# Performance work log

Hardware: AMD Instinct MI355X
Metric: run time of the kernel (lower is better)

## Reference

```python
import jax, jax.numpy as jnp
import numpy as np

WINDOW_SIZE = 11
SIGMA = 1.5
CHANNELS = 3
DATA_RANGE = 1.0


def _create_window(window_size, channel):
    x = np.arange(window_size) - window_size // 2
    g = np.exp(-(x ** 2) / (2.0 * SIGMA ** 2))
    g = g / g.sum()
    w2d = np.outer(g, g).astype(np.float32)  # [ws, ws]
    # depthwise kernel, OIHW with I=1, O=channel
    return jnp.asarray(np.broadcast_to(w2d, (channel, 1, window_size, window_size)).copy())


def _depthwise_conv(x, window, channel):
    # x: [B, C, H, W], window: [C, 1, ws, ws], VALID padding, groups=C
    return jax.lax.conv_general_dilated(
        x, window, window_strides=(1, 1), padding='VALID',
        dimension_numbers=('NCHW', 'OIHW', 'NCHW'),
        feature_group_count=channel)


def setup_inputs() -> dict:
    key = jax.random.key(0)
    k1, k2 = jax.random.split(key)
    img1 = jax.random.uniform(k1, (32, CHANNELS, 512, 512), dtype=jnp.float32)
    img2 = jax.random.uniform(k2, (32, CHANNELS, 512, 512), dtype=jnp.float32)
    return {"img1": img1, "img2": img2}


def reference(img1, img2):
    channel = img1.shape[1]
    window = _create_window(WINDOW_SIZE, channel).astype(img1.dtype)

    mu1 = _depthwise_conv(img1, window, channel)
    mu2 = _depthwise_conv(img2, window, channel)
    mu1_sq = mu1 * mu1
    mu2_sq = mu2 * mu2
    mu1_mu2 = mu1 * mu2

    sigma1_sq = _depthwise_conv(img1 * img1, window, channel) - mu1_sq
    sigma2_sq = _depthwise_conv(img2 * img2, window, channel) - mu2_sq
    sigma12 = _depthwise_conv(img1 * img2, window, channel) - mu1_mu2

    C1 = (0.01 * DATA_RANGE) ** 2
    C2 = (0.03 * DATA_RANGE) ** 2
    v1 = 2.0 * sigma12 + C2
    v2 = sigma1_sq + sigma2_sq + C2
    ssim_map = (2.0 * mu1_mu2 + C1) * v1 / ((mu1_sq + mu2_sq + C1) * v2)
    # mean over channel, height, width -> per-image SSIM [B]
    return ssim_map.mean(axis=(1, 2, 3))
```

## Files before the change

### kernel.cpp

```cpp
#include <hip/hip_runtime.h>
#include <math.h>

#define H 512
#define W 512
#define OUT_H 502
#define OUT_W 502
#define C1c 1.0e-4f
#define C2c 9.0e-4f

#define TH 111
#define NR 121
#define NCOLS 256
#define HALO 10
#define RING_W 266

__global__ __launch_bounds__(256, 4)
void ssim_kernel(const float* __restrict__ img1,
                 const float* __restrict__ img2,
                 float* __restrict__ out) {
    __shared__ float2 ring[2][RING_W];
    __shared__ float wsum[4];

    const int tid = threadIdx.x;

    float g[11];
    {
        float s = 0.f;
#pragma unroll
        for (int i = 0; i < 11; ++i) {
            float d = (float)(i - 5);
            g[i] = expf(-d * d * (1.0f / 4.5f));
            s += g[i];
        }
        float inv = 1.0f / s;
#pragma unroll
        for (int i = 0; i < 11; ++i) {
            g[i] *= inv;
            g[i] = __uint_as_float(__builtin_amdgcn_readfirstlane(__float_as_uint(g[i])));
        }
    }

    const int X0  = blockIdx.x * NCOLS;
    const int oyb = blockIdx.y * TH;
    const int Y0  = min(oyb, H - NR);
    const int plane = blockIdx.z;
    const size_t pbase = (size_t)plane * (H * W);
    const float* __restrict__ p1 = img1 + pbase;
    const float* __restrict__ p2 = img2 + pbase;

    const int gx = X0 + tid;
    const int hx = min(X0 + NCOLS + tid, W - 1);
    const bool colok = (gx < OUT_W);

    float a0[11], a1[11], a2[11], a3[11], a4[11];
#pragma unroll
    for (int i = 0; i < 11; ++i) { a0[i]=0.f; a1[i]=0.f; a2[i]=0.f; a3[i]=0.f; a4[i]=0.f; }

    float lsum = 0.f;

    int rowoff = Y0 * W;
    const int rowcap = (H - 1) * W;

    float va, vb, ha = 0.f, hb = 0.f;
    {
        const float* row1 = p1 + rowoff;
        const float* row2 = p2 + rowoff;
        va = row1[gx]; vb = row2[gx];
        if (tid < HALO) { ha = row1[hx]; hb = row2[hx]; }
    }

#pragma unroll 1
    for (int rb = 0; rb < NR; rb += 11) {
#pragma unroll
        for (int p = 0; p < 11; ++p) {
            const int r = rb + p;
            float2* rs = ring[r & 1];

            rs[tid] = make_float2(va, vb);
            if (tid < HALO) rs[NCOLS + tid] = make_float2(ha, hb);

            __syncthreads();

            rowoff = min(rowoff + W, rowcap);
            {
                const float* row1 = p1 + rowoff;
                const float* row2 = p2 + rowoff;
                va = row1[gx]; vb = row2[gx];
                if (tid < HALO) { ha = row1[hx]; hb = row2[hx]; }
            }

            float h0, h1, h2, h3, h4;
            {
                const float2* rp = rs + tid;
#pragma unroll
                for (int t = 0; t < 11; ++t) {
                    const float2 v = rp[t];
                    const float w = g[t];
                    const float q2 = v.x * v.x, q3 = v.y * v.y, q4 = v.x * v.y;
                    if (t == 0) {
                        h0 = w * v.x; h1 = w * v.y; h2 = w * q2; h3 = w * q3; h4 = w * q4;
                    } else {
                        h0 = fmaf(w, v.x, h0); h1 = fmaf(w, v.y, h1);
                        h2 = fmaf(w, q2, h2);  h3 = fmaf(w, q3, h3);
                        h4 = fmaf(w, q4, h4);
                    }
                }
            }

#pragma unroll
            for (int a = 0; a < 11; ++a) {
                const float w = g[(p - a + 11) % 11];
                if (a == p) {
                    a0[a] = w * h0; a1[a] = w * h1; a2[a] = w * h2;
                    a3[a] = w * h3; a4[a] = w * h4;
                } else {
                    a0[a] = fmaf(w, h0, a0[a]); a1[a] = fmaf(w, h1, a1[a]);
                    a2[a] = fmaf(w, h2, a2[a]); a3[a] = fmaf(w, h3, a3[a]);
                    a4[a] = fmaf(w, h4, a4[a]);
                }
            }

            if (r >= 10) {
                const int e = (p + 1) % 11;
                const int oy = Y0 + r - 10;
                if (oy >= oyb) {
                    const float m1 = a0[e], m2 = a1[e];
                    const float m1s = m1 * m1, m2s = m2 * m2, m12 = m1 * m2;
                    const float sig1  = a2[e] - m1s;
                    const float sig2  = a3[e] - m2s;
                    const float sig12 = a4[e] - m12;
                    const float num = (2.f * m12 + C1c) * (2.f * sig12 + C2c);
                    const float den = (m1s + m2s + C1c) * (sig1 + sig2 + C2c);
                    const float v = num * __builtin_amdgcn_rcpf(den);
                    if (colok) lsum += v;
                }
            }
        }
    }

#pragma unroll
    for (int off = 32; off > 0; off >>= 1) lsum += __shfl_down(lsum, off, 64);
    if ((tid & 63) == 0) wsum[tid >> 6] = lsum;
    __syncthreads();
    if (tid == 0) {
        const float inv_count = 1.0f / (3.0f * (float)OUT_H * (float)OUT_W);
        const float total = (wsum[0] + wsum[1] + wsum[2] + wsum[3]) * inv_count;
        atomicAdd(&out[plane / 3], total);
    }
}

__global__ void zero_out(float* out, int n) {
    int i = threadIdx.x + blockIdx.x * blockDim.x;
    if (i < n) out[i] = 0.f;
}

extern "C" void kernel_launch(void* const* d_in, const int* in_sizes, int n_in,
                              void* d_out, int out_size, void* d_ws, size_t ws_size,
                              hipStream_t stream) {
    const float* img1 = (const float*)d_in[0];
    const float* img2 = (const float*)d_in[1];
    float* out = (float*)d_out;

    zero_out<<<1, 64, 0, stream>>>(out, out_size);

    const int nplanes = in_sizes[0] / (H * W);
    dim3 grid(W / NCOLS,
              (OUT_H + TH - 1) / TH,
              nplanes);
    ssim_kernel<<<grid, 256, 0, stream>>>(img1, img2, out);
}
```

Measured before the change: 275.2 us.

## Give each wavefront a private staging row and drop block-wide barriers

Each of the four wavefronts now owns a 64-column strip with its own 10-column halo in a private shared-memory slot. This replaces the block-wide __syncthreads per row with wave-level barriers. The staged entries are float4 holding x, y, x*y and x*x, so the horizontal pass does fewer multiplies. The column mask becomes an fma. The cost is more redundant halo loads, with 10 halo lanes per wave instead of per block, and wider LDS reads per tap.

```diff
diff --git a/kernel.cpp b/kernel.cpp
--- a/kernel.cpp
+++ b/kernel.cpp
@@ -10,18 +10,20 @@
 
 #define TH 111
 #define NR 121
-#define NCOLS 256
 #define HALO 10
-#define RING_W 266
+#define SPAN 64
+#define SLOTW 76
 
 __global__ __launch_bounds__(256, 4)
 void ssim_kernel(const float* __restrict__ img1,
                  const float* __restrict__ img2,
                  float* __restrict__ out) {
-    __shared__ float2 ring[2][RING_W];
+    __shared__ float4 stg[4][SLOTW];
     __shared__ float wsum[4];
 
-    const int tid = threadIdx.x;
+    const int tid  = threadIdx.x;
+    const int wid  = tid >> 6;
+    const int lane = tid & 63;
 
     float g[11];
     {
@@ -40,17 +42,20 @@
         }
     }
 
-    const int X0  = blockIdx.x * NCOLS;
-    const int oyb = blockIdx.y * TH;
-    const int Y0  = min(oyb, H - NR);
+    const int base = blockIdx.x * 256 + wid * SPAN;
+    const int oyb  = blockIdx.y * TH;
+    const int Y0   = min(oyb, H - NR);
     const int plane = blockIdx.z;
     const size_t pbase = (size_t)plane * (H * W);
     const float* __restrict__ p1 = img1 + pbase;
     const float* __restrict__ p2 = img2 + pbase;
 
-    const int gx = X0 + tid;
-    const int hx = min(X0 + NCOLS + tid, W - 1);
-    const bool colok = (gx < OUT_W);
+    const int gx = base + lane;
+    const int hx = min(base + SPAN + lane, W - 1);
+    const float cmask = (gx < OUT_W) ? 1.0f : 0.0f;
+    const bool hl = (lane < HALO);
+
+    float4* const st = stg[wid];
 
     float a0[11], a1[11], a2[11], a3[11], a4[11];
 #pragma unroll
@@ -58,54 +63,50 @@
 
     float lsum = 0.f;
 
-    int rowoff = Y0 * W;
-    const int rowcap = (H - 1) * W;
+    int ro = Y0 * W;
+    const int rocap = (H - 1) * W;
 
-    float va, vb, ha = 0.f, hb = 0.f;
-    {
-        const float* row1 = p1 + rowoff;
-        const float* row2 = p2 + rowoff;
-        va = row1[gx]; vb = row2[gx];
-        if (tid < HALO) { ha = row1[hx]; hb = row2[hx]; }
-    }
+    float m1v = p1[ro + gx], m2v = p2[ro + gx];
+    float h1v = 0.f, h2v = 0.f;
+    if (hl) { h1v = p1[ro + hx]; h2v = p2[ro + hx]; }
 
 #pragma unroll 1
     for (int rb = 0; rb < NR; rb += 11) {
 #pragma unroll
         for (int p = 0; p < 11; ++p) {
             const int r = rb + p;
-            float2* rs = ring[r & 1];
 
-            rs[tid] = make_float2(va, vb);
-            if (tid < HALO) rs[NCOLS + tid] = make_float2(ha, hb);
+            st[lane] = make_float4(m1v, m2v, m1v * m2v, m1v * m1v);
+            if (hl) st[SPAN + lane] = make_float4(h1v, h2v, h1v * h2v, h1v * h1v);
 
-            __syncthreads();
+            ro = min(ro + W, rocap);
+            m1v = p1[ro + gx]; m2v = p2[ro + gx];
+            if (hl) { h1v = p1[ro + hx]; h2v = p2[ro + hx]; }
 
-            rowoff = min(rowoff + W, rowcap);
-            {
-                const float* row1 = p1 + rowoff;
-                const float* row2 = p2 + rowoff;
-                va = row1[gx]; vb = row2[gx];
-                if (tid < HALO) { ha = row1[hx]; hb = row2[hx]; }
-            }
+            __builtin_amdgcn_wave_barrier();
 
             float h0, h1, h2, h3, h4;
             {
-                const float2* rp = rs + tid;
+                const float4* rp = st + lane;
 #pragma unroll
                 for (int t = 0; t < 11; ++t) {
-                    const float2 v = rp[t];
+                    const float4 v = rp[t];
                     const float w = g[t];
-                    const float q2 = v.x * v.x, q3 = v.y * v.y, q4 = v.x * v.y;
+                    const float q22 = v.y * v.y;
                     if (t == 0) {
-                        h0 = w * v.x; h1 = w * v.y; h2 = w * q2; h3 = w * q3; h4 = w * q4;
+                        h0 = w * v.x; h1 = w * v.y; h2 = w * v.w;
+                        h3 = w * q22; h4 = w * v.z;
                     } else {
-                        h0 = fmaf(w, v.x, h0); h1 = fmaf(w, v.y, h1);
-                        h2 = fmaf(w, q2, h2);  h3 = fmaf(w, q3, h3);
-                        h4 = fmaf(w, q4, h4);
+                        h0 = fmaf(w, v.x, h0);
+                        h1 = fmaf(w, v.y, h1);
+                        h2 = fmaf(w, v.w, h2);
+                        h3 = fmaf(w, q22, h3);
+                        h4 = fmaf(w, v.z, h4);
                     }
                 }
             }
+
+            __builtin_amdgcn_wave_barrier();
 
 #pragma unroll
             for (int a = 0; a < 11; ++a) {
@@ -132,7 +133,7 @@
                     const float num = (2.f * m12 + C1c) * (2.f * sig12 + C2c);
                     const float den = (m1s + m2s + C1c) * (sig1 + sig2 + C2c);
                     const float v = num * __builtin_amdgcn_rcpf(den);
-                    if (colok) lsum += v;
+                    lsum = fmaf(cmask, v, lsum);
                 }
             }
         }
@@ -140,7 +141,7 @@
 
 #pragma unroll
     for (int off = 32; off > 0; off >>= 1) lsum += __shfl_down(lsum, off, 64);
-    if ((tid & 63) == 0) wsum[tid >> 6] = lsum;
+    if (lane == 0) wsum[wid] = lsum;
     __syncthreads();
     if (tid == 0) {
         const float inv_count = 1.0f / (3.0f * (float)OUT_H * (float)OUT_W);
@@ -164,7 +165,7 @@
     zero_out<<<1, 64, 0, stream>>>(out, out_size);
 
     const int nplanes = in_sizes[0] / (H * W);
-    dim3 grid(W / NCOLS,
+    dim3 grid(W / 256,
               (OUT_H + TH - 1) / TH,
               nplanes);
     ssim_kernel<<<grid, 256, 0, stream>>>(img1, img2, out);
```

Result: no change. 275.5 us (+0.1%).
